# Kernel optimization log

Hardware: AMD Instinct MI355X
Metric: run time of the kernel (lower is better)

## Reference

```python
import jax, jax.numpy as jnp
import numpy as np

N_NODES = 262144
N_EDGES = 4194304
NUM_GRAPHS = 1024
K = 2          # k clusters / particles
D = 4          # particle_latent_dim
D_Q = D // 2   # position part of latent


def setup_inputs() -> dict:
    key = jax.random.key(0)
    ks = jax.random.split(key, 20)
    w = lambda i, shape: 0.1 * jax.random.normal(ks[i], shape, jnp.float32)
    return {
        "x": jax.random.normal(ks[0], (N_NODES, 4), jnp.float32),
        "pos": jax.random.normal(ks[1], (N_NODES, 3), jnp.float32),
        "edge_index": jax.random.randint(ks[2], (2, N_EDGES), 0, N_NODES),
        "batch": jnp.sort(jax.random.randint(ks[3], (N_NODES,), 0, NUM_GRAPHS)),
        "enc_w1": w(4, (9, 16)), "enc_b1": jnp.zeros((16,), jnp.float32),
        "enc_w2": w(5, (16, 16)), "enc_b2": jnp.zeros((16,), jnp.float32),
        "pool_w": w(6, (16, K)), "pool_b": jnp.zeros((K,), jnp.float32),
        "toz_w": w(7, (16, D)), "toz_b": jnp.zeros((D,), jnp.float32),
        "vp_w1": w(8, (1, 32)), "vp_b1": jnp.zeros((32,), jnp.float32),
        "vp_w2": w(9, (32, 1)), "vp_b2": jnp.zeros((1,), jnp.float32),
        "bridge_w": w(10, (K * D, 8 * 4)), "bridge_b": jnp.zeros((8 * 4,), jnp.float32),
    }


def reference(x, pos, edge_index, batch,
              enc_w1, enc_b1, enc_w2, enc_b2,
              pool_w, pool_b, toz_w, toz_b,
              vp_w1, vp_b1, vp_w2, vp_b2,
              bridge_w, bridge_b):
    src = edge_index[0]  # j (source)
    dst = edge_index[1]  # i (target, PyG default flow)

    # --- EquiLayer: edge gather -> small MLP message -> mean scatter ---
    rel_pos = pos[src] - pos[dst]
    dist = jnp.linalg.norm(rel_pos, axis=-1, keepdims=True)       # [E,1]
    feat = jnp.concatenate([x[dst], x[src], dist], axis=-1)       # [E,9]
    msg = jax.nn.silu(feat @ enc_w1 + enc_b1) @ enc_w2 + enc_b2   # [E,16]
    agg = jax.ops.segment_sum(msg, dst, num_segments=N_NODES)     # [N,16]
    cnt = jax.ops.segment_sum(jnp.ones((msg.shape[0], 1), msg.dtype), dst,
                              num_segments=N_NODES)
    h = jax.nn.relu(agg / jnp.maximum(cnt, 1.0))                  # [N,16]

    # --- softmax-weighted scatter pooling over graphs ---
    s = jax.nn.softmax(h @ pool_w + pool_b, axis=-1)              # [N,K]
    weighted = s[:, :, None] * h[:, None, :]                      # [N,K,16]
    pooled = jax.ops.segment_sum(weighted, batch, num_segments=NUM_GRAPHS)  # [B,K,16]
    z = pooled @ toz_w + toz_b                                    # [B,K,D]

    # --- decode ---
    recon = (z.reshape(z.shape[0], -1) @ bridge_w + bridge_b).reshape(-1, 8, 4)

    # --- pairwise potential + forces on position part of latent ---
    iu0, iu1 = np.triu_indices(K, 1)

    def potential(q):
        diff = q[:, :, None, :] - q[:, None, :, :]
        d = jnp.sqrt(jnp.sum(diff * diff, axis=-1) + 1e-6)        # [B,K,K]
        d_flat = d[:, iu0, iu1][..., None]                        # [B,P,1]
        v = jax.nn.softplus(d_flat @ vp_w1 + vp_b1) @ vp_w2 + vp_b2
        return v.sum(axis=1)                                      # [B,1]

    q = z[..., :D_Q]
    V = potential(q)
    forces = -jax.grad(lambda qq: potential(qq).sum())(q)
    return recon, z, s, forces, V
```

## Files before the change

### kernel.cpp

```cpp
#include <hip/hip_runtime.h>
#include <math.h>

#define N_NODES   262144
#define N_EDGES   4194304
#define NUM_GRAPHS 1024
#define NBKT      256
#define BNODE     1024
#define CAPK      17408
#define NBLK      256
#define EPB       16384
#define SEGCAP    112

typedef _Float16 h8 __attribute__((ext_vector_type(8)));

static __device__ __forceinline__ float fast_rcp(float v) {
    return __builtin_amdgcn_rcpf(v);
}

__global__ __launch_bounds__(1024) void bin_pack_kernel(
    const int* __restrict__ ei, const float* __restrict__ x,
    const float* __restrict__ pos,
    int* __restrict__ cnts, int* __restrict__ staged,
    h8* __restrict__ xp, float* __restrict__ pooled)
{
    __shared__ int cnt[NBKT], rcnt[NBKT], lbase[NBKT];
    __shared__ int wsum[4];
    __shared__ int stage[EPB];
    int tid = threadIdx.x;
    if (tid < NBKT) { cnt[tid] = 0; rcnt[tid] = 0; }
    __syncthreads();

    {
        int n0 = blockIdx.x * 1024 + tid;
        float4 xv = *(const float4*)(x + 4*n0);
        h8 o;
        o[0] = (_Float16)xv.x; o[1] = (_Float16)xv.y;
        o[2] = (_Float16)xv.z; o[3] = (_Float16)xv.w;
        o[4] = (_Float16)pos[3*n0+0]; o[5] = (_Float16)pos[3*n0+1];
        o[6] = (_Float16)pos[3*n0+2]; o[7] = (_Float16)0.0f;
        xp[n0] = o;
        if (blockIdx.x < 32) pooled[blockIdx.x*1024 + tid] = 0.0f;
    }

    int base = blockIdx.x * EPB;
    const int4* d4 = (const int4*)(ei + N_EDGES + base);
    const int4* s4 = (const int4*)(ei + base);
    int4 dv[4];
    #pragma unroll
    for (int i = 0; i < 4; ++i) {
        dv[i] = d4[i*1024 + tid];
        atomicAdd(&cnt[dv[i].x >> 10], 1);
        atomicAdd(&cnt[dv[i].y >> 10], 1);
        atomicAdd(&cnt[dv[i].z >> 10], 1);
        atomicAdd(&cnt[dv[i].w >> 10], 1);
    }
    __syncthreads();

    int lane = tid & 63, wid = tid >> 6;
    if (tid < NBKT) {
        int inc = cnt[tid];
        #pragma unroll
        for (int o = 1; o < 64; o <<= 1) {
            int t = __shfl_up(inc, o);
            if (lane >= o) inc += t;
        }
        if (lane == 63) wsum[wid] = inc;
        cnt[tid] = inc;
    }
    __syncthreads();
    if (tid < NBKT) {
        int inc  = cnt[tid];
        int prev = __shfl_up(inc, 1);
        int excl = (lane == 0) ? 0 : prev;
        int wb = 0;
        #pragma unroll
        for (int w = 0; w < 4; ++w) if (w < wid) wb += wsum[w];
        lbase[tid] = wb + excl;
    }
    __syncthreads();

    #pragma unroll
    for (int i = 0; i < 4; ++i) {
        int4 sv = s4[i*1024 + tid];
        int d, s, bk, r;
        d = dv[i].x; s = sv.x; bk = d >> 10; r = atomicAdd(&rcnt[bk], 1);
        stage[lbase[bk] + r] = ((d & 1023) << 18) | s;
        d = dv[i].y; s = sv.y; bk = d >> 10; r = atomicAdd(&rcnt[bk], 1);
        stage[lbase[bk] + r] = ((d & 1023) << 18) | s;
        d = dv[i].z; s = sv.z; bk = d >> 10; r = atomicAdd(&rcnt[bk], 1);
        stage[lbase[bk] + r] = ((d & 1023) << 18) | s;
        d = dv[i].w; s = sv.w; bk = d >> 10; r = atomicAdd(&rcnt[bk], 1);
        stage[lbase[bk] + r] = ((d & 1023) << 18) | s;
    }
    __syncthreads();

    int sub = tid & 31, grp = tid >> 5;
    #pragma unroll
    for (int pass = 0; pass < NBKT/32; ++pass) {
        int bk  = pass*32 + grp;
        int c2  = rcnt[bk];
        int lb  = lbase[bk];
        if (c2 > SEGCAP) c2 = SEGCAP;
        size_t sb = ((size_t)bk*NBLK + blockIdx.x)*SEGCAP;
        for (int k = sub; k < c2; k += 32)
            staged[sb + k] = stage[lb + k];
        if (sub == 0) cnts[bk*NBLK + blockIdx.x] = c2;
    }
}

static __device__ __forceinline__ void edge_contrib(
    const float* __restrict__ sw1, const float* __restrict__ hd,
    float4 xs, float dist, float* __restrict__ acc)
{
    float h[16];
    #pragma unroll
    for (int j4 = 0; j4 < 4; ++j4) {
        float4 w = *(const float4*)&sw1[4*16 + 4*j4];
        h[4*j4+0] = fmaf(xs.x, w.x, hd[4*j4+0]);
        h[4*j4+1] = fmaf(xs.x, w.y, hd[4*j4+1]);
        h[4*j4+2] = fmaf(xs.x, w.z, hd[4*j4+2]);
        h[4*j4+3] = fmaf(xs.x, w.w, hd[4*j4+3]);
    }
    #pragma unroll
    for (int j4 = 0; j4 < 4; ++j4) {
        float4 w = *(const float4*)&sw1[5*16 + 4*j4];
        h[4*j4+0] = fmaf(xs.y, w.x, h[4*j4+0]);
        h[4*j4+1] = fmaf(xs.y, w.y, h[4*j4+1]);
        h[4*j4+2] = fmaf(xs.y, w.z, h[4*j4+2]);
        h[4*j4+3] = fmaf(xs.y, w.w, h[4*j4+3]);
    }
    #pragma unroll
    for (int j4 = 0; j4 < 4; ++j4) {
        float4 w = *(const float4*)&sw1[6*16 + 4*j4];
        h[4*j4+0] = fmaf(xs.z, w.x, h[4*j4+0]);
        h[4*j4+1] = fmaf(xs.z, w.y, h[4*j4+1]);
        h[4*j4+2] = fmaf(xs.z, w.z, h[4*j4+2]);
        h[4*j4+3] = fmaf(xs.z, w.w, h[4*j4+3]);
    }
    #pragma unroll
    for (int j4 = 0; j4 < 4; ++j4) {
        float4 w = *(const float4*)&sw1[7*16 + 4*j4];
        h[4*j4+0] = fmaf(xs.w, w.x, h[4*j4+0]);
        h[4*j4+1] = fmaf(xs.w, w.y, h[4*j4+1]);
        h[4*j4+2] = fmaf(xs.w, w.z, h[4*j4+2]);
        h[4*j4+3] = fmaf(xs.w, w.w, h[4*j4+3]);
    }
    #pragma unroll
    for (int j4 = 0; j4 < 4; ++j4) {
        float4 w = *(const float4*)&sw1[8*16 + 4*j4];
        h[4*j4+0] = fmaf(dist, w.x, h[4*j4+0]);
        h[4*j4+1] = fmaf(dist, w.y, h[4*j4+1]);
        h[4*j4+2] = fmaf(dist, w.z, h[4*j4+2]);
        h[4*j4+3] = fmaf(dist, w.w, h[4*j4+3]);
    }
    #pragma unroll
    for (int j = 0; j < 16; ++j) {
        float sg = fast_rcp(1.0f + __expf(-h[j]));
        acc[j] = fmaf(h[j], sg, acc[j]);
    }
}

__global__ __launch_bounds__(1024, 4) void fused_node_kernel(
    const h8* __restrict__ xp,
    const int* __restrict__ cnts, const int* __restrict__ staged,
    const int* __restrict__ batch,
    const float* __restrict__ w1, const float* __restrict__ b1,
    const float* __restrict__ w2, const float* __restrict__ b2,
    const float* __restrict__ pw, const float* __restrict__ pb,
    float* __restrict__ s_out, float* __restrict__ pooled)
{
    __shared__ int esrc[CAPK];
    __shared__ int ldeg[BNODE];
    __shared__ int scnt[NBLK];
    __shared__ int wsum[16];
    __shared__ __align__(16) float sw1[144];
    __shared__ float sb1[16];
    __shared__ __align__(16) float sw2[256];
    __shared__ float sb2[16];
    __shared__ float spw[32];
    __shared__ float spb[2];

    int tid = threadIdx.x;
    int bkt = blockIdx.x;
    if (tid < 144) sw1[tid] = w1[tid];
    if (tid >= 144 && tid < 160) sb1[tid - 144] = b1[tid - 144];
    if (tid >= 160 && tid < 176) sb2[tid - 160] = b2[tid - 160];
    if (tid >= 176 && tid < 208) spw[tid - 176] = pw[tid - 176];
    if (tid >= 208 && tid < 210) spb[tid - 208] = pb[tid - 208];
    if (tid >= 256 && tid < 512) sw2[tid - 256] = w2[tid - 256];
    if (tid >= 512 && tid < 768) scnt[tid - 512] = cnts[bkt*NBLK + (tid - 512)];
    ldeg[tid] = 0;
    __syncthreads();

    int lane = tid & 63, wid = tid >> 6;
    int nb0  = bkt * BNODE;

    for (int s = wid; s < NBLK; s += 16) {
        int c = scnt[s];
        const int* seg = staged + ((size_t)bkt*NBLK + s)*SEGCAP;
        for (int i = lane; i < c; i += 64)
            atomicAdd(&ldeg[seg[i] >> 18], 1);
    }
    __syncthreads();

    int dg  = ldeg[tid];
    int inc = dg;
    #pragma unroll
    for (int o = 1; o < 64; o <<= 1) {
        int t = __shfl_up(inc, o);
        if (lane >= o) inc += t;
    }
    if (lane == 63) wsum[wid] = inc;
    __syncthreads();
    int wb = 0;
    #pragma unroll
    for (int w = 0; w < 16; ++w) if (w < wid) wb += wsum[w];
    int r0 = wb + inc - dg;
    ldeg[tid] = r0;
    __syncthreads();

    for (int s = wid; s < NBLK; s += 16) {
        int c = scnt[s];
        const int* seg = staged + ((size_t)bkt*NBLK + s)*SEGCAP;
        for (int i = lane; i < c; i += 64) {
            int p = seg[i];
            int r = atomicAdd(&ldeg[p >> 18], 1);
            if (r < CAPK) esrc[r] = p & 0x3FFFF;
        }
    }
    __syncthreads();

    int n = nb0 + tid;
    h8 rd = xp[n];
    float4 xd = make_float4((float)rd[0], (float)rd[1], (float)rd[2], (float)rd[3]);
    float pdx = (float)rd[4], pdy = (float)rd[5], pdz = (float)rd[6];

    float hd[16];
    #pragma unroll
    for (int j = 0; j < 16; ++j) hd[j] = sb1[j];
    #pragma unroll
    for (int j4 = 0; j4 < 4; ++j4) {
        float4 w0 = *(const float4*)&sw1[0*16 + 4*j4];
        float4 w1r = *(const float4*)&sw1[1*16 + 4*j4];
        float4 w2r = *(const float4*)&sw1[2*16 + 4*j4];
        float4 w3r = *(const float4*)&sw1[3*16 + 4*j4];
        hd[4*j4+0] = fmaf(xd.x, w0.x, hd[4*j4+0]);
        hd[4*j4+1] = fmaf(xd.x, w0.y, hd[4*j4+1]);
        hd[4*j4+2] = fmaf(xd.x, w0.z, hd[4*j4+2]);
        hd[4*j4+3] = fmaf(xd.x, w0.w, hd[4*j4+3]);
        hd[4*j4+0] = fmaf(xd.y, w1r.x, hd[4*j4+0]);
        hd[4*j4+1] = fmaf(xd.y, w1r.y, hd[4*j4+1]);
        hd[4*j4+2] = fmaf(xd.y, w1r.z, hd[4*j4+2]);
        hd[4*j4+3] = fmaf(xd.y, w1r.w, hd[4*j4+3]);
        hd[4*j4+0] = fmaf(xd.z, w2r.x, hd[4*j4+0]);
        hd[4*j4+1] = fmaf(xd.z, w2r.y, hd[4*j4+1]);
        hd[4*j4+2] = fmaf(xd.z, w2r.z, hd[4*j4+2]);
        hd[4*j4+3] = fmaf(xd.z, w2r.w, hd[4*j4+3]);
        hd[4*j4+0] = fmaf(xd.w, w3r.x, hd[4*j4+0]);
        hd[4*j4+1] = fmaf(xd.w, w3r.y, hd[4*j4+1]);
        hd[4*j4+2] = fmaf(xd.w, w3r.z, hd[4*j4+2]);
        hd[4*j4+3] = fmaf(xd.w, w3r.w, hd[4*j4+3]);
    }

    float acc[16];
    #pragma unroll
    for (int j = 0; j < 16; ++j) acc[j] = 0.0f;

    int k = 0;
    for (; k + 2 <= dg; k += 2) {
        int s0 = esrc[r0 + k];
        int s1 = esrc[r0 + k + 1];
        h8 e0 = xp[s0];
        h8 e1 = xp[s1];

        float4 a0 = make_float4((float)e0[0], (float)e0[1], (float)e0[2], (float)e0[3]);
        float dx0 = (float)e0[4] - pdx, dy0 = (float)e0[5] - pdy, dz0 = (float)e0[6] - pdz;
        float dist0 = sqrtf(fmaf(dx0, dx0, fmaf(dy0, dy0, dz0*dz0)));
        edge_contrib(sw1, hd, a0, dist0, acc);

        float4 a1 = make_float4((float)e1[0], (float)e1[1], (float)e1[2], (float)e1[3]);
        float dx1 = (float)e1[4] - pdx, dy1 = (float)e1[5] - pdy, dz1 = (float)e1[6] - pdz;
        float dist1 = sqrtf(fmaf(dx1, dx1, fmaf(dy1, dy1, dz1*dz1)));
        edge_contrib(sw1, hd, a1, dist1, acc);
    }
    if (k < dg) {
        int s0 = esrc[r0 + k];
        h8 e0 = xp[s0];
        float4 a0 = make_float4((float)e0[0], (float)e0[1], (float)e0[2], (float)e0[3]);
        float dx0 = (float)e0[4] - pdx, dy0 = (float)e0[5] - pdy, dz0 = (float)e0[6] - pdz;
        float dist0 = sqrtf(fmaf(dx0, dx0, fmaf(dy0, dy0, dz0*dz0)));
        edge_contrib(sw1, hd, a0, dist0, acc);
    }

    float c = (float)dg;
    float inv = fast_rcp(fmaxf(c, 1.0f));
    float h[16];
    #pragma unroll
    for (int j = 0; j < 16; ++j) h[j] = c * sb2[j];
    #pragma unroll
    for (int i = 0; i < 16; ++i) {
        float f = acc[i];
        #pragma unroll
        for (int j4 = 0; j4 < 4; ++j4) {
            float4 w = *(const float4*)&sw2[i*16 + 4*j4];
            h[4*j4+0] = fmaf(f, w.x, h[4*j4+0]);
            h[4*j4+1] = fmaf(f, w.y, h[4*j4+1]);
            h[4*j4+2] = fmaf(f, w.z, h[4*j4+2]);
            h[4*j4+3] = fmaf(f, w.w, h[4*j4+3]);
        }
    }
    #pragma unroll
    for (int j = 0; j < 16; ++j) h[j] = fmaxf(h[j] * inv, 0.0f);

    float l0 = spb[0], l1 = spb[1];
    #pragma unroll
    for (int j = 0; j < 16; ++j) {
        l0 = fmaf(h[j], spw[2*j+0], l0);
        l1 = fmaf(h[j], spw[2*j+1], l1);
    }
    float m = fmaxf(l0, l1);
    float e0 = __expf(l0 - m), e1 = __expf(l1 - m);
    float r = fast_rcp(e0 + e1);
    float s0 = e0 * r, s1 = e1 * r;
    s_out[2*n+0] = s0;
    s_out[2*n+1] = s1;

    float w[32];
    #pragma unroll
    for (int j = 0; j < 16; ++j) { w[j] = s0 * h[j]; w[16+j] = s1 * h[j]; }

    int b = batch[n];
    #pragma unroll
    for (int o = 1; o < 64; o <<= 1) {
        int bn = __shfl_down(b, o);
        bool take = (lane + o < 64) && (bn == b);
        #pragma unroll
        for (int cc = 0; cc < 32; ++cc) {
            float vn = __shfl_down(w[cc], o);
            if (take) w[cc] += vn;
        }
    }
    int bp = __shfl_up(b, 1);
    if (lane == 0 || bp != b) {
        float* pg = pooled + 32*b;
        #pragma unroll
        for (int cc = 0; cc < 32; ++cc) unsafeAtomicAdd(pg + cc, w[cc]);
    }
}

__global__ __launch_bounds__(256) void graph_kernel(
    const float* __restrict__ pooled,
    const float* __restrict__ toz_w, const float* __restrict__ toz_b,
    const float* __restrict__ vp_w1, const float* __restrict__ vp_b1,
    const float* __restrict__ vp_w2, const float* __restrict__ vp_b2,
    const float* __restrict__ bridge_w, const float* __restrict__ bridge_b,
    float* __restrict__ out_recon, float* __restrict__ out_z,
    float* __restrict__ out_forces, float* __restrict__ out_V)
{
    int g = blockIdx.x * 256 + threadIdx.x;
    if (g >= NUM_GRAPHS) return;

    const float* P = pooled + 32*g;
    float z[8];
    #pragma unroll
    for (int k = 0; k < 2; ++k) {
        #pragma unroll
        for (int d = 0; d < 4; ++d) {
            float a = toz_b[d];
            #pragma unroll
            for (int i = 0; i < 16; ++i) a = fmaf(P[16*k+i], toz_w[4*i+d], a);
            z[4*k+d] = a;
        }
    }
    #pragma unroll
    for (int i = 0; i < 8; ++i) out_z[8*g+i] = z[i];

    #pragma unroll
    for (int j = 0; j < 32; ++j) {
        float a = bridge_b[j];
        #pragma unroll
        for (int i = 0; i < 8; ++i) a = fmaf(z[i], bridge_w[32*i+j], a);
        out_recon[32*g+j] = a;
    }

    float d0 = z[0]-z[4], d1 = z[1]-z[5];
    float dd = sqrtf(d0*d0 + d1*d1 + 1e-6f);

    float V = vp_b2[0];
    float dV = 0.0f;
    #pragma unroll
    for (int j = 0; j < 32; ++j) {
        float w1 = vp_w1[j];
        float t  = fmaf(dd, w1, vp_b1[j]);
        float et = __expf(t);
        float sp = __logf(1.0f + et);
        float sg = et / (1.0f + et);
        float w2 = vp_w2[j];
        V  = fmaf(sp, w2, V);
        dV = fmaf(sg * w1, w2, dV);
    }
    out_V[g] = V;

    float scale = dV / dd;
    float gx = scale * d0, gy = scale * d1;
    out_forces[4*g+0] = -gx;
    out_forces[4*g+1] = -gy;
    out_forces[4*g+2] =  gx;
    out_forces[4*g+3] =  gy;
}

extern "C" void kernel_launch(void* const* d_in, const int* in_sizes, int n_in,
                              void* d_out, int out_size, void* d_ws, size_t ws_size,
                              hipStream_t stream) {
    const float* x        = (const float*)d_in[0];
    const float* pos      = (const float*)d_in[1];
    const int*   ei       = (const int*)  d_in[2];
    const int*   batch    = (const int*)  d_in[3];
    const float* enc_w1   = (const float*)d_in[4];
    const float* enc_b1   = (const float*)d_in[5];
    const float* enc_w2   = (const float*)d_in[6];
    const float* enc_b2   = (const float*)d_in[7];
    const float* pool_w   = (const float*)d_in[8];
    const float* pool_b   = (const float*)d_in[9];
    const float* toz_w    = (const float*)d_in[10];
    const float* toz_b    = (const float*)d_in[11];
    const float* vp_w1    = (const float*)d_in[12];
    const float* vp_b1    = (const float*)d_in[13];
    const float* vp_w2    = (const float*)d_in[14];
    const float* vp_b2    = (const float*)d_in[15];
    const float* bridge_w = (const float*)d_in[16];
    const float* bridge_b = (const float*)d_in[17];

    int*   cnts   = (int*)d_ws;
    float* pooled = (float*)d_ws + NBKT*NBLK;
    int*   staged = (int*)d_ws + NBKT*NBLK + 32768;
    h8*    xp     = (h8*)(staged + (size_t)NBKT*NBLK*SEGCAP);

    float* out        = (float*)d_out;
    float* out_recon  = out;
    float* out_z      = out_recon + 1024*32;
    float* out_s      = out_z + 1024*8;
    float* out_forces = out_s + (size_t)N_NODES*2;
    float* out_V      = out_forces + 1024*4;

    bin_pack_kernel<<<NBLK, 1024, 0, stream>>>(ei, x, pos, cnts, staged, xp, pooled);
    fused_node_kernel<<<NBKT, 1024, 0, stream>>>(
        xp, cnts, staged, batch,
        enc_w1, enc_b1, enc_w2, enc_b2, pool_w, pool_b, out_s, pooled);
    graph_kernel<<<NUM_GRAPHS/256, 256, 0, stream>>>(
        pooled, toz_w, toz_b, vp_w1, vp_b1, vp_w2, vp_b2,
        bridge_w, bridge_b, out_recon, out_z, out_forces, out_V);
}
```

Before: 212.1 us.

## Sort nodes by degree within block to balance per-wavefront edge loops

Builds a per-block degree histogram and counting-sort permutation so each thread processes a node of similar in-degree to its wavefront neighbours. This targets divergence in the edge gather loop, where a wave waits on its highest-degree node. Per-node accumulators are passed back through a new shared-memory buffer so the second-layer MLP and pooling still run in original node order. The change adds roughly 70KB of LDS per block plus extra barriers and atomics, which may reduce how many blocks fit on a CU.

```diff
diff --git a/kernel.cpp b/kernel.cpp
--- a/kernel.cpp
+++ b/kernel.cpp
@@ -169,10 +169,14 @@
     const float* __restrict__ pw, const float* __restrict__ pb,
     float* __restrict__ s_out, float* __restrict__ pooled)
 {
-    __shared__ int esrc[CAPK];
-    __shared__ int ldeg[BNODE];
-    __shared__ int scnt[NBLK];
-    __shared__ int wsum[16];
+    __shared__ int   esrc[CAPK];
+    __shared__ float accbuf[BNODE*17];
+    __shared__ int   ldeg[BNODE];
+    __shared__ int   rofs[BNODE];
+    __shared__ int   perm[BNODE];
+    __shared__ int   scnt[NBLK];
+    __shared__ int   dhist[64];
+    __shared__ int   wsum[16];
     __shared__ __align__(16) float sw1[144];
     __shared__ float sb1[16];
     __shared__ __align__(16) float sw2[256];
@@ -189,6 +193,7 @@
     if (tid >= 208 && tid < 210) spb[tid - 208] = pb[tid - 208];
     if (tid >= 256 && tid < 512) sw2[tid - 256] = w2[tid - 256];
     if (tid >= 512 && tid < 768) scnt[tid - 512] = cnts[bkt*NBLK + (tid - 512)];
+    if (tid >= 768 && tid < 832) dhist[tid - 768] = 0;
     ldeg[tid] = 0;
     __syncthreads();
 
@@ -216,6 +221,7 @@
     #pragma unroll
     for (int w = 0; w < 16; ++w) if (w < wid) wb += wsum[w];
     int r0 = wb + inc - dg;
+    rofs[tid] = r0;
     ldeg[tid] = r0;
     __syncthreads();
 
@@ -228,10 +234,29 @@
             if (r < CAPK) esrc[r] = p & 0x3FFFF;
         }
     }
-    __syncthreads();
-
-    int n = nb0 + tid;
-    h8 rd = xp[n];
+    int db = dg < 63 ? dg : 63;
+    atomicAdd(&dhist[db], 1);
+    __syncthreads();
+
+    if (tid < 64) {
+        int c  = dhist[tid];
+        int i2 = c;
+        #pragma unroll
+        for (int o = 1; o < 64; o <<= 1) {
+            int t2 = __shfl_up(i2, o);
+            if (lane >= o) i2 += t2;
+        }
+        dhist[tid] = i2 - c;
+    }
+    __syncthreads();
+    int rank = atomicAdd(&dhist[db], 1);
+    perm[rank] = tid;
+    __syncthreads();
+
+    int v   = perm[tid];
+    int r0v = rofs[v];
+    int dgv = ldeg[v] - r0v;
+    h8 rd = xp[nb0 + v];
     float4 xd = make_float4((float)rd[0], (float)rd[1], (float)rd[2], (float)rd[3]);
     float pdx = (float)rd[4], pdy = (float)rd[5], pdz = (float)rd[6];
 
@@ -267,9 +292,9 @@
     for (int j = 0; j < 16; ++j) acc[j] = 0.0f;
 
     int k = 0;
-    for (; k + 2 <= dg; k += 2) {
-        int s0 = esrc[r0 + k];
-        int s1 = esrc[r0 + k + 1];
+    for (; k + 2 <= dgv; k += 2) {
+        int s0 = esrc[r0v + k];
+        int s1 = esrc[r0v + k + 1];
         h8 e0 = xp[s0];
         h8 e1 = xp[s1];
 
@@ -283,8 +308,8 @@
         float dist1 = sqrtf(fmaf(dx1, dx1, fmaf(dy1, dy1, dz1*dz1)));
         edge_contrib(sw1, hd, a1, dist1, acc);
     }
-    if (k < dg) {
-        int s0 = esrc[r0 + k];
+    if (k < dgv) {
+        int s0 = esrc[r0v + k];
         h8 e0 = xp[s0];
         float4 a0 = make_float4((float)e0[0], (float)e0[1], (float)e0[2], (float)e0[3]);
         float dx0 = (float)e0[4] - pdx, dy0 = (float)e0[5] - pdy, dz0 = (float)e0[6] - pdz;
@@ -292,14 +317,20 @@
         edge_contrib(sw1, hd, a0, dist0, acc);
     }
 
-    float c = (float)dg;
+    #pragma unroll
+    for (int j = 0; j < 16; ++j) accbuf[v*17 + j] = acc[j];
+    __syncthreads();
+
+    int n = nb0 + tid;
+    int dgc = ldeg[tid] - rofs[tid];
+    float c = (float)dgc;
     float inv = fast_rcp(fmaxf(c, 1.0f));
     float h[16];
     #pragma unroll
     for (int j = 0; j < 16; ++j) h[j] = c * sb2[j];
     #pragma unroll
     for (int i = 0; i < 16; ++i) {
-        float f = acc[i];
+        float f = accbuf[tid*17 + i];
         #pragma unroll
         for (int j4 = 0; j4 < 4; ++j4) {
             float4 w = *(const float4*)&sw2[i*16 + 4*j4];
```

New measurement: 208.8 us. About the same (-1.5%).
